# Kernel tuning notes

Hardware: AMD Instinct MI355X
Metric: run time of the kernel (lower is better)

## Reference

```python
import jax, jax.numpy as jnp
import numpy as np

T, D_MODEL, D_FF, N_EXPERTS, TOPK = 4096, 2048, 8192, 8, 2


def setup_inputs() -> dict:
    key = jax.random.key(0)
    k1, k2, k3, k4 = jax.random.split(key, 4)
    x = jax.random.normal(k1, (T, D_MODEL), dtype=jnp.float32)
    gating_output = jax.random.normal(k2, (T, N_EXPERTS), dtype=jnp.float32)
    # gate_proj and up_proj concatenated along output dim: [E, 2*d_ff, d_model]
    gate_up_proj = jax.random.normal(k3, (N_EXPERTS, 2 * D_FF, D_MODEL), dtype=jnp.float32) * 0.02
    # down_proj: [E, d_model, d_ff]
    down_proj = jax.random.normal(k4, (N_EXPERTS, D_MODEL, D_FF), dtype=jnp.float32) * 0.02
    return {"x": x, "gating_output": gating_output, "gate_up_proj": gate_up_proj,
            "down_proj": down_proj, "topk": TOPK}


def reference(x, gating_output, gate_up_proj, down_proj, topk):
    n_experts = gate_up_proj.shape[0]
    d_ff = down_proj.shape[2]
    # Router: fp32 softmax over experts, top-k, renormalize over the k selected.
    probs = jax.nn.softmax(gating_output.astype(jnp.float32), axis=1)  # [T, E]
    routing_weights, selected_experts = jax.lax.top_k(probs, topk)     # [T, k]
    routing_weights = routing_weights / jnp.sum(routing_weights, axis=-1, keepdims=True)
    routing_weights = routing_weights.astype(x.dtype)
    # Expert MLPs: silu(x @ Wg^T) * (x @ Wu^T) @ Wd^T, combined by routing weight.
    out = jnp.zeros_like(x)
    for e in range(n_experts):  # small fixed expert count
        coef = jnp.sum(jnp.where(selected_experts == e, routing_weights, 0.0), axis=-1)  # [T]
        gu = x @ gate_up_proj[e].T                     # [T, 2*d_ff]
        h = jax.nn.silu(gu[:, :d_ff]) * gu[:, d_ff:]   # [T, d_ff]
        out = out + coef[:, None] * (h @ down_proj[e].T)  # [T, d_model]
    return out
```

## Files before the change

### kernel.cpp

```cpp
#include <hip/hip_runtime.h>
#include <hip/hip_bf16.h>
#include <cstdint>
#include <cstddef>

#define T_TOK 4096
#define DMODEL 2048
#define DFF 8192
#define NEXP 8
#define NPAIR (T_TOK * 2)

typedef __bf16 bf16_t;
typedef __bf16 bf16x8 __attribute__((ext_vector_type(8)));
typedef float fx4 __attribute__((ext_vector_type(4)));

__device__ __forceinline__ void gload16(const bf16_t* src, bf16_t* dst) {
    __builtin_amdgcn_global_load_lds(
        (const __attribute__((address_space(1))) uint32_t*)(src),
        (__attribute__((address_space(3))) uint32_t*)(dst), 16, 0, 0);
}

__device__ __forceinline__ bf16x8 pack8(const fx4 lo, const fx4 hi) {
    bf16x8 o;
    o[0] = (bf16_t)lo[0]; o[1] = (bf16_t)lo[1]; o[2] = (bf16_t)lo[2]; o[3] = (bf16_t)lo[3];
    o[4] = (bf16_t)hi[0]; o[5] = (bf16_t)hi[1]; o[6] = (bf16_t)hi[2]; o[7] = (bf16_t)hi[3];
    return o;
}

__global__ void router_kernel(const float* __restrict__ gating, int* __restrict__ counts,
                              int* __restrict__ tok_list, float* __restrict__ w_list) {
    int t = blockIdx.x * blockDim.x + threadIdx.x;
    if (t >= T_TOK) return;
    float l[NEXP];
    float mx = -1e30f;
#pragma unroll
    for (int e = 0; e < NEXP; e++) { l[e] = gating[t * NEXP + e]; mx = fmaxf(mx, l[e]); }
#pragma unroll
    for (int e = 0; e < NEXP; e++) { l[e] = __expf(l[e] - mx); }
    int e0 = 0; float p0 = l[0];
#pragma unroll
    for (int e = 1; e < NEXP; e++) { if (l[e] > p0) { p0 = l[e]; e0 = e; } }
    int e1 = -1; float p1 = -1.0f;
#pragma unroll
    for (int e = 0; e < NEXP; e++) { if (e != e0 && l[e] > p1) { p1 = l[e]; e1 = e; } }
    float inv = 1.0f / (p0 + p1);
    int s0 = atomicAdd(&counts[e0], 1);
    tok_list[e0 * T_TOK + s0] = t; w_list[e0 * T_TOK + s0] = p0 * inv;
    int s1 = atomicAdd(&counts[e1], 1);
    tok_list[e1 * T_TOK + s1] = t; w_list[e1 * T_TOK + s1] = p1 * inv;
}

__global__ void scan_kernel(const int* __restrict__ counts, int* __restrict__ offsets) {
    if (threadIdx.x == 0 && blockIdx.x == 0) {
        int acc = 0;
        for (int e = 0; e < NEXP; e++) { offsets[e] = acc; acc += counts[e]; }
        offsets[NEXP] = acc;
    }
}

__global__ void cvt_x_kernel(const float* __restrict__ x, bf16_t* __restrict__ xb) {
    int i = blockIdx.x * blockDim.x + threadIdx.x;
    const fx4* src = (const fx4*)x;
    fx4 v0 = src[2 * i], v1 = src[2 * i + 1];
    *(bf16x8*)(xb + (size_t)i * 8) = pack8(v0, v1);
}

__global__ __launch_bounds__(512, 4) void gateup_kernel(
    const bf16_t* __restrict__ xb, const float* __restrict__ gup,
    const int* __restrict__ counts, const int* __restrict__ offsets,
    const int* __restrict__ tok_list, bf16_t* __restrict__ h_buf)
{
    const int idx = blockIdx.x;
    const int q = idx & 7;
    const int mslot = (idx >> 3) & 15;
    const int g2 = idx >> 7;
    const int e = g2 >> 4;
    const int cnt = counts[e];
    const int mbase = mslot * 256;
    if (mbase >= cnt) return;
    const int y = q + 8 * (g2 & 15);
    const int nb = y * 64;
    const int off_e = offsets[e];

    __shared__ __align__(16) bf16_t lds_a[256 * 64];
    __shared__ __align__(16) bf16_t lds_w[128 * 64];

    const int tid = threadIdx.x;
    const int lane = tid & 63;
    const int w = tid >> 6;
    const int wm = (w >> 1) * 64;
    const int wc = (w & 1);

    const bf16_t* a_src[4];
    int a_doff[4];
#pragma unroll
    for (int j = 0; j < 4; j++) {
        int row = (w * 4 + j) * 8 + (lane >> 3);
        int cs = (lane & 7) ^ (row & 7);
        int slot = mbase + row;
        int tok = tok_list[e * T_TOK + (slot < cnt ? slot : cnt - 1)];
        a_src[j] = xb + (size_t)tok * DMODEL + cs * 8;
        a_doff[j] = (w * 4 + j) * 512;
    }
    const float* w_src[2];
    int w_st[2];
    const float* gup_e = gup + (size_t)e * (2 * DFF) * DMODEL;
#pragma unroll
    for (int t = 0; t < 2; t++) {
        int cid = t * 512 + tid;
        int row = cid >> 3, c = cid & 7;
        int grow = (row < 64) ? (nb + row) : (DFF + nb + (row - 64));
        w_src[t] = gup_e + (size_t)grow * DMODEL + c * 8;
        w_st[t] = row * 64 + ((c ^ (row & 7)) * 8);
    }

    fx4 accg[4][2] = {};
    fx4 accu[4][2] = {};

    for (int k0 = 0; k0 < DMODEL; k0 += 64) {
#pragma unroll
        for (int j = 0; j < 4; j++) gload16(a_src[j] + k0, &lds_a[a_doff[j]]);
#pragma unroll
        for (int t = 0; t < 2; t++) {
            fx4 lo = *(const fx4*)(w_src[t] + k0);
            fx4 hi = *(const fx4*)(w_src[t] + k0 + 4);
            *(bf16x8*)(&lds_w[w_st[t]]) = pack8(lo, hi);
        }
        __syncthreads();
#pragma unroll
        for (int kp = 0; kp < 2; kp++) {
            const int ke = kp * 4 + (lane >> 4);
            bf16x8 af[4], gf[2], uf[2];
#pragma unroll
            for (int m = 0; m < 4; m++) {
                int r = wm + m * 16 + (lane & 15);
                af[m] = *(const bf16x8*)(&lds_a[r * 64 + ((ke ^ (r & 7)) * 8)]);
            }
#pragma unroll
            for (int n = 0; n < 2; n++) {
                int r = wc * 32 + n * 16 + (lane & 15);
                gf[n] = *(const bf16x8*)(&lds_w[r * 64 + ((ke ^ (r & 7)) * 8)]);
                uf[n] = *(const bf16x8*)(&lds_w[(r + 64) * 64 + ((ke ^ (r & 7)) * 8)]);
            }
#pragma unroll
            for (int m = 0; m < 4; m++)
#pragma unroll
                for (int n = 0; n < 2; n++) {
                    accg[m][n] = __builtin_amdgcn_mfma_f32_16x16x32_bf16(af[m], gf[n], accg[m][n], 0, 0, 0);
                    accu[m][n] = __builtin_amdgcn_mfma_f32_16x16x32_bf16(af[m], uf[n], accu[m][n], 0, 0, 0);
                }
        }
        __syncthreads();
    }

    const int colbase = nb + wc * 32 + (lane & 15);
#pragma unroll
    for (int m = 0; m < 4; m++) {
        int rb = wm + m * 16 + ((lane >> 4) * 4);
#pragma unroll
        for (int j = 0; j < 4; j++) {
            int slot = mbase + rb + j;
            if (slot < cnt) {
                size_t hrow = (size_t)(off_e + slot);
#pragma unroll
                for (int n = 0; n < 2; n++) {
                    float g = accg[m][n][j];
                    float u = accu[m][n][j];
                    float hv = g * u / (1.0f + __expf(-g));
                    h_buf[hrow * DFF + colbase + n * 16] = (bf16_t)hv;
                }
            }
        }
    }
}

__global__ __launch_bounds__(512, 4) void down_kernel(
    const bf16_t* __restrict__ h_buf, const float* __restrict__ dwn,
    const int* __restrict__ counts, const int* __restrict__ offsets,
    const int* __restrict__ tok_list, const float* __restrict__ w_list,
    float* __restrict__ out)
{
    const int idx = blockIdx.x;
    const int q = idx & 7;
    const int mslot = (idx >> 3) & 15;
    const int rest = idx >> 7;
    const int pp = rest & 1;
    const int e = rest >> 1;
    const int cnt = counts[e];
    const int mbase = mslot * 256;
    if (mbase >= cnt) return;
    const int y = q + 8 * pp;
    const int nbase = y * 128;
    const int off_e = offsets[e];

    __shared__ __align__(16) bf16_t lds_a[256 * 64];
    __shared__ __align__(16) bf16_t lds_w[128 * 64];

    const int tid = threadIdx.x;
    const int lane = tid & 63;
    const int w = tid >> 6;
    const int wm = (w >> 1) * 64;
    const int wn = (w & 1) * 64;

    const bf16_t* a_src[4];
    int a_doff[4];
#pragma unroll
    for (int j = 0; j < 4; j++) {
        int row = (w * 4 + j) * 8 + (lane >> 3);
        int cs = (lane & 7) ^ (row & 7);
        int slot = mbase + row;
        int hrow = off_e + (slot < cnt ? slot : cnt - 1);
        a_src[j] = h_buf + (size_t)hrow * DFF + cs * 8;
        a_doff[j] = (w * 4 + j) * 512;
    }
    const float* w_src[2];
    int w_st[2];
    const float* dwn_e = dwn + (size_t)e * DMODEL * DFF;
#pragma unroll
    for (int t = 0; t < 2; t++) {
        int cid = t * 512 + tid;
        int row = cid >> 3, c = cid & 7;
        w_src[t] = dwn_e + (size_t)(nbase + row) * DFF + c * 8;
        w_st[t] = row * 64 + ((c ^ (row & 7)) * 8);
    }

    fx4 acc[4][4] = {};

    for (int k0 = 0; k0 < DFF; k0 += 64) {
#pragma unroll
        for (int j = 0; j < 4; j++) gload16(a_src[j] + k0, &lds_a[a_doff[j]]);
#pragma unroll
        for (int t = 0; t < 2; t++) {
            fx4 lo = *(const fx4*)(w_src[t] + k0);
            fx4 hi = *(const fx4*)(w_src[t] + k0 + 4);
            *(bf16x8*)(&lds_w[w_st[t]]) = pack8(lo, hi);
        }
        __syncthreads();
#pragma unroll
        for (int kp = 0; kp < 2; kp++) {
            const int ke = kp * 4 + (lane >> 4);
            bf16x8 af[4], bfr[4];
#pragma unroll
            for (int m = 0; m < 4; m++) {
                int r = wm + m * 16 + (lane & 15);
                af[m] = *(const bf16x8*)(&lds_a[r * 64 + ((ke ^ (r & 7)) * 8)]);
            }
#pragma unroll
            for (int n = 0; n < 4; n++) {
                int r = wn + n * 16 + (lane & 15);
                bfr[n] = *(const bf16x8*)(&lds_w[r * 64 + ((ke ^ (r & 7)) * 8)]);
            }
#pragma unroll
            for (int m = 0; m < 4; m++)
#pragma unroll
                for (int n = 0; n < 4; n++)
                    acc[m][n] = __builtin_amdgcn_mfma_f32_16x16x32_bf16(af[m], bfr[n], acc[m][n], 0, 0, 0);
        }
        __syncthreads();
    }

    const int colb = nbase + wn + (lane & 15);
#pragma unroll
    for (int m = 0; m < 4; m++) {
        int rb = wm + m * 16 + ((lane >> 4) * 4);
#pragma unroll
        for (int j = 0; j < 4; j++) {
            int slot = mbase + rb + j;
            if (slot < cnt) {
                int tok = tok_list[e * T_TOK + slot];
                float wgt = w_list[e * T_TOK + slot];
#pragma unroll
                for (int n = 0; n < 4; n++)
                    atomicAdd(&out[(size_t)tok * DMODEL + colb + n * 16], wgt * acc[m][n][j]);
            }
        }
    }
}

extern "C" void kernel_launch(void* const* d_in, const int* in_sizes, int n_in,
                              void* d_out, int out_size, void* d_ws, size_t ws_size,
                              hipStream_t stream) {
    const float* x      = (const float*)d_in[0];
    const float* gating = (const float*)d_in[1];
    const float* gup    = (const float*)d_in[2];
    const float* dwn    = (const float*)d_in[3];
    float* out = (float*)d_out;

    char* ws = (char*)d_ws;
    int*    counts   = (int*)(ws + 0);
    int*    offsets  = (int*)(ws + 64);
    int*    tok_list = (int*)(ws + 128);
    float*  w_list   = (float*)(ws + 128 + 131072);
    bf16_t* xb       = (bf16_t*)(ws + 262400);
    bf16_t* h_buf    = (bf16_t*)(ws + 17039872);

    hipMemsetAsync(counts, 0, 64, stream);
    hipMemsetAsync(out, 0, (size_t)out_size * sizeof(float), stream);

    router_kernel<<<dim3(T_TOK / 256), dim3(256), 0, stream>>>(gating, counts, tok_list, w_list);
    scan_kernel<<<dim3(1), dim3(64), 0, stream>>>(counts, offsets);
    cvt_x_kernel<<<dim3(T_TOK * DMODEL / 8 / 256), dim3(256), 0, stream>>>(x, xb);

    gateup_kernel<<<dim3(16384), dim3(512), 0, stream>>>(
        xb, gup, counts, offsets, tok_list, h_buf);

    down_kernel<<<dim3(2048), dim3(512), 0, stream>>>(
        h_buf, dwn, counts, offsets, tok_list, w_list, out);
}
```

Baseline: 1.442 ms.

## Double-buffer LDS tiles and halve M-tile to 128 rows in MoE GEMMs

Both expert GEMM kernels now use 256-thread blocks with a 128-row M tile, and twice the blocks are launched. They ping-pong between two LDS buffers: the next k-tile's weights are prefetched into registers and the activations sent to LDS asynchronously while MFMAs run on the current tile. This is meant to hide global-load latency and cut one barrier per k-step. The cost is that each weight tile, converted from fp32, is now re-read by twice as many M-blocks, and register pressure rises from the prefetch buffers.

```diff
diff --git a/kernel.cpp b/kernel.cpp
--- a/kernel.cpp
+++ b/kernel.cpp
@@ -64,25 +64,25 @@
     *(bf16x8*)(xb + (size_t)i * 8) = pack8(v0, v1);
 }
 
-__global__ __launch_bounds__(512, 4) void gateup_kernel(
+__global__ __launch_bounds__(256, 2) void gateup_kernel(
     const bf16_t* __restrict__ xb, const float* __restrict__ gup,
     const int* __restrict__ counts, const int* __restrict__ offsets,
     const int* __restrict__ tok_list, bf16_t* __restrict__ h_buf)
 {
     const int idx = blockIdx.x;
     const int q = idx & 7;
-    const int mslot = (idx >> 3) & 15;
-    const int g2 = idx >> 7;
+    const int mslot = (idx >> 3) & 31;
+    const int g2 = idx >> 8;
     const int e = g2 >> 4;
     const int cnt = counts[e];
-    const int mbase = mslot * 256;
+    const int mbase = mslot * 128;
     if (mbase >= cnt) return;
     const int y = q + 8 * (g2 & 15);
     const int nb = y * 64;
     const int off_e = offsets[e];
 
-    __shared__ __align__(16) bf16_t lds_a[256 * 64];
-    __shared__ __align__(16) bf16_t lds_w[128 * 64];
+    __shared__ __align__(16) bf16_t lds_a[2][128 * 64];
+    __shared__ __align__(16) bf16_t lds_w[2][128 * 64];
 
     const int tid = threadIdx.x;
     const int lane = tid & 63;
@@ -101,31 +101,53 @@
         a_src[j] = xb + (size_t)tok * DMODEL + cs * 8;
         a_doff[j] = (w * 4 + j) * 512;
     }
-    const float* w_src[2];
-    int w_st[2];
+    const float* w_src[4];
+    int w_st[4];
     const float* gup_e = gup + (size_t)e * (2 * DFF) * DMODEL;
 #pragma unroll
-    for (int t = 0; t < 2; t++) {
-        int cid = t * 512 + tid;
+    for (int c4 = 0; c4 < 4; c4++) {
+        int cid = c4 * 256 + tid;
         int row = cid >> 3, c = cid & 7;
         int grow = (row < 64) ? (nb + row) : (DFF + nb + (row - 64));
-        w_src[t] = gup_e + (size_t)grow * DMODEL + c * 8;
-        w_st[t] = row * 64 + ((c ^ (row & 7)) * 8);
+        w_src[c4] = gup_e + (size_t)grow * DMODEL + c * 8;
+        w_st[c4] = row * 64 + ((c ^ (row & 7)) * 8);
     }
 
     fx4 accg[4][2] = {};
     fx4 accu[4][2] = {};
 
-    for (int k0 = 0; k0 < DMODEL; k0 += 64) {
-#pragma unroll
-        for (int j = 0; j < 4; j++) gload16(a_src[j] + k0, &lds_a[a_doff[j]]);
-#pragma unroll
-        for (int t = 0; t < 2; t++) {
-            fx4 lo = *(const fx4*)(w_src[t] + k0);
-            fx4 hi = *(const fx4*)(w_src[t] + k0 + 4);
-            *(bf16x8*)(&lds_w[w_st[t]]) = pack8(lo, hi);
-        }
+    {
+        fx4 wr[8];
+#pragma unroll
+        for (int c4 = 0; c4 < 4; c4++) {
+            wr[2 * c4]     = *(const fx4*)(w_src[c4]);
+            wr[2 * c4 + 1] = *(const fx4*)(w_src[c4] + 4);
+        }
+#pragma unroll
+        for (int j = 0; j < 4; j++) gload16(a_src[j], &lds_a[0][a_doff[j]]);
+#pragma unroll
+        for (int c4 = 0; c4 < 4; c4++)
+            *(bf16x8*)(&lds_w[0][w_st[c4]]) = pack8(wr[2 * c4], wr[2 * c4 + 1]);
         __syncthreads();
+    }
+
+    const int NT = DMODEL / 64;
+    for (int t = 0; t < NT; ++t) {
+        const int cur = t & 1;
+        const int nxt = cur ^ 1;
+        fx4 wr[8];
+        if (t + 1 < NT) {
+#pragma unroll
+            for (int c4 = 0; c4 < 4; c4++) {
+                wr[2 * c4]     = *(const fx4*)(w_src[c4] + (t + 1) * 64);
+                wr[2 * c4 + 1] = *(const fx4*)(w_src[c4] + (t + 1) * 64 + 4);
+            }
+#pragma unroll
+            for (int j = 0; j < 4; j++)
+                gload16(a_src[j] + (t + 1) * 64, &lds_a[nxt][a_doff[j]]);
+        }
+        const bf16_t* A = lds_a[cur];
+        const bf16_t* W = lds_w[cur];
 #pragma unroll
         for (int kp = 0; kp < 2; kp++) {
             const int ke = kp * 4 + (lane >> 4);
@@ -133,13 +155,13 @@
 #pragma unroll
             for (int m = 0; m < 4; m++) {
                 int r = wm + m * 16 + (lane & 15);
-                af[m] = *(const bf16x8*)(&lds_a[r * 64 + ((ke ^ (r & 7)) * 8)]);
+                af[m] = *(const bf16x8*)(&A[r * 64 + ((ke ^ (r & 7)) * 8)]);
             }
 #pragma unroll
             for (int n = 0; n < 2; n++) {
                 int r = wc * 32 + n * 16 + (lane & 15);
-                gf[n] = *(const bf16x8*)(&lds_w[r * 64 + ((ke ^ (r & 7)) * 8)]);
-                uf[n] = *(const bf16x8*)(&lds_w[(r + 64) * 64 + ((ke ^ (r & 7)) * 8)]);
+                gf[n] = *(const bf16x8*)(&W[r * 64 + ((ke ^ (r & 7)) * 8)]);
+                uf[n] = *(const bf16x8*)(&W[(r + 64) * 64 + ((ke ^ (r & 7)) * 8)]);
             }
 #pragma unroll
             for (int m = 0; m < 4; m++)
@@ -148,6 +170,11 @@
                     accg[m][n] = __builtin_amdgcn_mfma_f32_16x16x32_bf16(af[m], gf[n], accg[m][n], 0, 0, 0);
                     accu[m][n] = __builtin_amdgcn_mfma_f32_16x16x32_bf16(af[m], uf[n], accu[m][n], 0, 0, 0);
                 }
+        }
+        if (t + 1 < NT) {
+#pragma unroll
+            for (int c4 = 0; c4 < 4; c4++)
+                *(bf16x8*)(&lds_w[nxt][w_st[c4]]) = pack8(wr[2 * c4], wr[2 * c4 + 1]);
         }
         __syncthreads();
     }
@@ -173,7 +200,7 @@
     }
 }
 
-__global__ __launch_bounds__(512, 4) void down_kernel(
+__global__ __launch_bounds__(256, 2) void down_kernel(
     const bf16_t* __restrict__ h_buf, const float* __restrict__ dwn,
     const int* __restrict__ counts, const int* __restrict__ offsets,
     const int* __restrict__ tok_list, const float* __restrict__ w_list,
@@ -181,19 +208,19 @@
 {
     const int idx = blockIdx.x;
     const int q = idx & 7;
-    const int mslot = (idx >> 3) & 15;
-    const int rest = idx >> 7;
+    const int mslot = (idx >> 3) & 31;
+    const int rest = idx >> 8;
     const int pp = rest & 1;
     const int e = rest >> 1;
     const int cnt = counts[e];
-    const int mbase = mslot * 256;
+    const int mbase = mslot * 128;
     if (mbase >= cnt) return;
     const int y = q + 8 * pp;
     const int nbase = y * 128;
     const int off_e = offsets[e];
 
-    __shared__ __align__(16) bf16_t lds_a[256 * 64];
-    __shared__ __align__(16) bf16_t lds_w[128 * 64];
+    __shared__ __align__(16) bf16_t lds_a[2][128 * 64];
+    __shared__ __align__(16) bf16_t lds_w[2][128 * 64];
 
     const int tid = threadIdx.x;
     const int lane = tid & 63;
@@ -212,29 +239,51 @@
         a_src[j] = h_buf + (size_t)hrow * DFF + cs * 8;
         a_doff[j] = (w * 4 + j) * 512;
     }
-    const float* w_src[2];
-    int w_st[2];
+    const float* w_src[4];
+    int w_st[4];
     const float* dwn_e = dwn + (size_t)e * DMODEL * DFF;
 #pragma unroll
-    for (int t = 0; t < 2; t++) {
-        int cid = t * 512 + tid;
+    for (int c4 = 0; c4 < 4; c4++) {
+        int cid = c4 * 256 + tid;
         int row = cid >> 3, c = cid & 7;
-        w_src[t] = dwn_e + (size_t)(nbase + row) * DFF + c * 8;
-        w_st[t] = row * 64 + ((c ^ (row & 7)) * 8);
+        w_src[c4] = dwn_e + (size_t)(nbase + row) * DFF + c * 8;
+        w_st[c4] = row * 64 + ((c ^ (row & 7)) * 8);
     }
 
     fx4 acc[4][4] = {};
 
-    for (int k0 = 0; k0 < DFF; k0 += 64) {
-#pragma unroll
-        for (int j = 0; j < 4; j++) gload16(a_src[j] + k0, &lds_a[a_doff[j]]);
-#pragma unroll
-        for (int t = 0; t < 2; t++) {
-            fx4 lo = *(const fx4*)(w_src[t] + k0);
-            fx4 hi = *(const fx4*)(w_src[t] + k0 + 4);
-            *(bf16x8*)(&lds_w[w_st[t]]) = pack8(lo, hi);
-        }
+    {
+        fx4 wr[8];
+#pragma unroll
+        for (int c4 = 0; c4 < 4; c4++) {
+            wr[2 * c4]     = *(const fx4*)(w_src[c4]);
+            wr[2 * c4 + 1] = *(const fx4*)(w_src[c4] + 4);
+        }
+#pragma unroll
+        for (int j = 0; j < 4; j++) gload16(a_src[j], &lds_a[0][a_doff[j]]);
+#pragma unroll
+        for (int c4 = 0; c4 < 4; c4++)
+            *(bf16x8*)(&lds_w[0][w_st[c4]]) = pack8(wr[2 * c4], wr[2 * c4 + 1]);
         __syncthreads();
+    }
+
+    const int NT = DFF / 64;
+    for (int t = 0; t < NT; ++t) {
+        const int cur = t & 1;
+        const int nxt = cur ^ 1;
+        fx4 wr[8];
+        if (t + 1 < NT) {
+#pragma unroll
+            for (int c4 = 0; c4 < 4; c4++) {
+                wr[2 * c4]     = *(const fx4*)(w_src[c4] + (t + 1) * 64);
+                wr[2 * c4 + 1] = *(const fx4*)(w_src[c4] + (t + 1) * 64 + 4);
+            }
+#pragma unroll
+            for (int j = 0; j < 4; j++)
+                gload16(a_src[j] + (t + 1) * 64, &lds_a[nxt][a_doff[j]]);
+        }
+        const bf16_t* A = lds_a[cur];
+        const bf16_t* W = lds_w[cur];
 #pragma unroll
         for (int kp = 0; kp < 2; kp++) {
             const int ke = kp * 4 + (lane >> 4);
@@ -242,18 +291,23 @@
 #pragma unroll
             for (int m = 0; m < 4; m++) {
                 int r = wm + m * 16 + (lane & 15);
-                af[m] = *(const bf16x8*)(&lds_a[r * 64 + ((ke ^ (r & 7)) * 8)]);
+                af[m] = *(const bf16x8*)(&A[r * 64 + ((ke ^ (r & 7)) * 8)]);
             }
 #pragma unroll
             for (int n = 0; n < 4; n++) {
                 int r = wn + n * 16 + (lane & 15);
-                bfr[n] = *(const bf16x8*)(&lds_w[r * 64 + ((ke ^ (r & 7)) * 8)]);
+                bfr[n] = *(const bf16x8*)(&W[r * 64 + ((ke ^ (r & 7)) * 8)]);
             }
 #pragma unroll
             for (int m = 0; m < 4; m++)
 #pragma unroll
                 for (int n = 0; n < 4; n++)
                     acc[m][n] = __builtin_amdgcn_mfma_f32_16x16x32_bf16(af[m], bfr[n], acc[m][n], 0, 0, 0);
+        }
+        if (t + 1 < NT) {
+#pragma unroll
+            for (int c4 = 0; c4 < 4; c4++)
+                *(bf16x8*)(&lds_w[nxt][w_st[c4]]) = pack8(wr[2 * c4], wr[2 * c4 + 1]);
         }
         __syncthreads();
     }
@@ -300,9 +354,9 @@
     scan_kernel<<<dim3(1), dim3(64), 0, stream>>>(counts, offsets);
     cvt_x_kernel<<<dim3(T_TOK * DMODEL / 8 / 256), dim3(256), 0, stream>>>(x, xb);
 
-    gateup_kernel<<<dim3(16384), dim3(512), 0, stream>>>(
+    gateup_kernel<<<dim3(32768), dim3(256), 0, stream>>>(
         xb, gup, counts, offsets, tok_list, h_buf);
 
-    down_kernel<<<dim3(2048), dim3(512), 0, stream>>>(
+    down_kernel<<<dim3(4096), dim3(256), 0, stream>>>(
         h_buf, dwn, counts, offsets, tok_list, w_list, out);
 }
```

New measurement: 1.849 ms. 28.2% more time.

## Pre-convert expert weights to bf16 and use async LDS loads in GEMMs

Applied to the files above, without the earlier changes.

Adds a kernel that converts the fp32 gate/up and down weights to bf16 in workspace on every call. New GEMM kernels then stream the bf16 weights straight into LDS with global_load_lds, using 128-row M tiles and 256-thread blocks instead of 256-row tiles and 512 threads. The aim is to drop the in-loop fp32 weight conversion and simplify the load path. In exchange, each call pays an extra full read and write of the weights. The new path runs only when the workspace is large enough; otherwise the old fp32 kernels are kept as a fallback.

```diff
diff --git a/kernel.cpp b/kernel.cpp
--- a/kernel.cpp
+++ b/kernel.cpp
@@ -64,7 +64,226 @@
     *(bf16x8*)(xb + (size_t)i * 8) = pack8(v0, v1);
 }
 
-__global__ __launch_bounds__(512, 4) void gateup_kernel(
+__global__ void wcvt_kernel(const float* __restrict__ src, bf16_t* __restrict__ dst, int nchunk) {
+    int stride = gridDim.x * blockDim.x;
+    for (int i = blockIdx.x * blockDim.x + threadIdx.x; i < nchunk; i += stride) {
+        const fx4* s = (const fx4*)src + 2 * (size_t)i;
+        fx4 v0 = s[0], v1 = s[1];
+        *(bf16x8*)(dst + (size_t)i * 8) = pack8(v0, v1);
+    }
+}
+
+__global__ __launch_bounds__(256, 4) void gateup_kernel(
+    const bf16_t* __restrict__ xb, const bf16_t* __restrict__ wg,
+    const int* __restrict__ counts, const int* __restrict__ offsets,
+    const int* __restrict__ tok_list, bf16_t* __restrict__ h_buf)
+{
+    const int idx = blockIdx.x;
+    const int q = idx & 7;
+    const int mslot = (idx >> 3) & 31;
+    const int g2 = idx >> 8;
+    const int e = g2 >> 4;
+    const int cnt = counts[e];
+    const int mbase = mslot * 128;
+    if (mbase >= cnt) return;
+    const int y = q + 8 * (g2 & 15);
+    const int nb = y * 64;
+    const int off_e = offsets[e];
+
+    __shared__ __align__(16) bf16_t lds_a[128 * 64];
+    __shared__ __align__(16) bf16_t lds_w[128 * 64];
+
+    const int tid = threadIdx.x;
+    const int lane = tid & 63;
+    const int w = tid >> 6;
+    const int wm = (w >> 1) * 64;
+    const int wc = (w & 1);
+    const int l15 = lane & 15;
+    const int l4 = lane >> 4;
+
+    const bf16_t* a_src[4];
+    int a_doff[4];
+#pragma unroll
+    for (int j = 0; j < 4; j++) {
+        int row = (w * 4 + j) * 8 + (lane >> 3);
+        int c8 = (lane & 7) ^ (row & 7);
+        int slot = mbase + row;
+        int tok = tok_list[e * T_TOK + (slot < cnt ? slot : cnt - 1)];
+        a_src[j] = xb + (size_t)tok * DMODEL + c8 * 8;
+        a_doff[j] = (w * 4 + j) * 512;
+    }
+    const bf16_t* w_src[4];
+    int w_doff[4];
+    const bf16_t* wg_e = wg + (size_t)e * (2 * DFF) * DMODEL;
+#pragma unroll
+    for (int j = 0; j < 4; j++) {
+        int row = (w * 4 + j) * 8 + (lane >> 3);
+        int c8 = (lane & 7) ^ (row & 7);
+        int grow = (row < 64) ? (nb + row) : (DFF + nb + (row - 64));
+        w_src[j] = wg_e + (size_t)grow * DMODEL + c8 * 8;
+        w_doff[j] = (w * 4 + j) * 512;
+    }
+
+    fx4 accg[4][2] = {};
+    fx4 accu[4][2] = {};
+
+    for (int k0 = 0; k0 < DMODEL; k0 += 64) {
+#pragma unroll
+        for (int j = 0; j < 4; j++) {
+            gload16(a_src[j] + k0, &lds_a[a_doff[j]]);
+            gload16(w_src[j] + k0, &lds_w[w_doff[j]]);
+        }
+        __syncthreads();
+#pragma unroll
+        for (int kp = 0; kp < 2; kp++) {
+            const int ke = kp * 4 + l4;
+            bf16x8 af[4], gf[2], uf[2];
+#pragma unroll
+            for (int m = 0; m < 4; m++) {
+                int r = wm + m * 16 + l15;
+                af[m] = *(const bf16x8*)(&lds_a[r * 64 + ((ke ^ (r & 7)) * 8)]);
+            }
+#pragma unroll
+            for (int n = 0; n < 2; n++) {
+                int r = wc * 32 + n * 16 + l15;
+                gf[n] = *(const bf16x8*)(&lds_w[r * 64 + ((ke ^ (r & 7)) * 8)]);
+                uf[n] = *(const bf16x8*)(&lds_w[(r + 64) * 64 + (((ke) ^ ((r + 64) & 7)) * 8)]);
+            }
+#pragma unroll
+            for (int m = 0; m < 4; m++)
+#pragma unroll
+                for (int n = 0; n < 2; n++) {
+                    accg[m][n] = __builtin_amdgcn_mfma_f32_16x16x32_bf16(af[m], gf[n], accg[m][n], 0, 0, 0);
+                    accu[m][n] = __builtin_amdgcn_mfma_f32_16x16x32_bf16(af[m], uf[n], accu[m][n], 0, 0, 0);
+                }
+        }
+        __syncthreads();
+    }
+
+    const int colbase = nb + wc * 32 + l15;
+#pragma unroll
+    for (int m = 0; m < 4; m++) {
+        int rb = wm + m * 16 + l4 * 4;
+#pragma unroll
+        for (int j = 0; j < 4; j++) {
+            int slot = mbase + rb + j;
+            if (slot < cnt) {
+                size_t hrow = (size_t)(off_e + slot);
+#pragma unroll
+                for (int n = 0; n < 2; n++) {
+                    float g = accg[m][n][j];
+                    float u = accu[m][n][j];
+                    float hv = g * u / (1.0f + __expf(-g));
+                    h_buf[hrow * DFF + colbase + n * 16] = (bf16_t)hv;
+                }
+            }
+        }
+    }
+}
+
+__global__ __launch_bounds__(256, 4) void down_kernel(
+    const bf16_t* __restrict__ h_buf, const bf16_t* __restrict__ wd,
+    const int* __restrict__ counts, const int* __restrict__ offsets,
+    const int* __restrict__ tok_list, const float* __restrict__ w_list,
+    float* __restrict__ out)
+{
+    const int idx = blockIdx.x;
+    const int q = idx & 7;
+    const int mslot = (idx >> 3) & 31;
+    const int rest = idx >> 8;
+    const int pp = rest & 1;
+    const int e = rest >> 1;
+    const int cnt = counts[e];
+    const int mbase = mslot * 128;
+    if (mbase >= cnt) return;
+    const int y = q + 8 * pp;
+    const int nbase = y * 128;
+    const int off_e = offsets[e];
+
+    __shared__ __align__(16) bf16_t lds_a[128 * 64];
+    __shared__ __align__(16) bf16_t lds_w[128 * 64];
+
+    const int tid = threadIdx.x;
+    const int lane = tid & 63;
+    const int w = tid >> 6;
+    const int wm = (w >> 1) * 64;
+    const int wn = (w & 1) * 64;
+    const int l15 = lane & 15;
+    const int l4 = lane >> 4;
+
+    const bf16_t* a_src[4];
+    int a_doff[4];
+#pragma unroll
+    for (int j = 0; j < 4; j++) {
+        int row = (w * 4 + j) * 8 + (lane >> 3);
+        int c8 = (lane & 7) ^ (row & 7);
+        int slot = mbase + row;
+        int hrow = off_e + (slot < cnt ? slot : cnt - 1);
+        a_src[j] = h_buf + (size_t)hrow * DFF + c8 * 8;
+        a_doff[j] = (w * 4 + j) * 512;
+    }
+    const bf16_t* w_src[4];
+    int w_doff[4];
+    const bf16_t* wd_e = wd + (size_t)e * DMODEL * DFF;
+#pragma unroll
+    for (int j = 0; j < 4; j++) {
+        int row = (w * 4 + j) * 8 + (lane >> 3);
+        int c8 = (lane & 7) ^ (row & 7);
+        w_src[j] = wd_e + (size_t)(nbase + row) * DFF + c8 * 8;
+        w_doff[j] = (w * 4 + j) * 512;
+    }
+
+    fx4 acc[4][4] = {};
+
+    for (int k0 = 0; k0 < DFF; k0 += 64) {
+#pragma unroll
+        for (int j = 0; j < 4; j++) {
+            gload16(a_src[j] + k0, &lds_a[a_doff[j]]);
+            gload16(w_src[j] + k0, &lds_w[w_doff[j]]);
+        }
+        __syncthreads();
+#pragma unroll
+        for (int kp = 0; kp < 2; kp++) {
+            const int ke = kp * 4 + l4;
+            bf16x8 af[4], bfr[4];
+#pragma unroll
+            for (int m = 0; m < 4; m++) {
+                int r = wm + m * 16 + l15;
+                af[m] = *(const bf16x8*)(&lds_a[r * 64 + ((ke ^ (r & 7)) * 8)]);
+            }
+#pragma unroll
+            for (int n = 0; n < 4; n++) {
+                int r = wn + n * 16 + l15;
+                bfr[n] = *(const bf16x8*)(&lds_w[r * 64 + ((ke ^ (r & 7)) * 8)]);
+            }
+#pragma unroll
+            for (int m = 0; m < 4; m++)
+#pragma unroll
+                for (int n = 0; n < 4; n++)
+                    acc[m][n] = __builtin_amdgcn_mfma_f32_16x16x32_bf16(af[m], bfr[n], acc[m][n], 0, 0, 0);
+        }
+        __syncthreads();
+    }
+
+    const int colb = nbase + wn + l15;
+#pragma unroll
+    for (int m = 0; m < 4; m++) {
+        int rb = wm + m * 16 + l4 * 4;
+#pragma unroll
+        for (int j = 0; j < 4; j++) {
+            int slot = mbase + rb + j;
+            if (slot < cnt) {
+                int tok = tok_list[e * T_TOK + slot];
+                float wgt = w_list[e * T_TOK + slot];
+#pragma unroll
+                for (int n = 0; n < 4; n++)
+                    atomicAdd(&out[(size_t)tok * DMODEL + colb + n * 16], wgt * acc[m][n][j]);
+            }
+        }
+    }
+}
+
+__global__ __launch_bounds__(512, 4) void gateup_f32_kernel(
     const bf16_t* __restrict__ xb, const float* __restrict__ gup,
     const int* __restrict__ counts, const int* __restrict__ offsets,
     const int* __restrict__ tok_list, bf16_t* __restrict__ h_buf)
@@ -173,7 +392,7 @@
     }
 }
 
-__global__ __launch_bounds__(512, 4) void down_kernel(
+__global__ __launch_bounds__(512, 4) void down_f32_kernel(
     const bf16_t* __restrict__ h_buf, const float* __restrict__ dwn,
     const int* __restrict__ counts, const int* __restrict__ offsets,
     const int* __restrict__ tok_list, const float* __restrict__ w_list,
@@ -292,6 +511,9 @@
     float*  w_list   = (float*)(ws + 128 + 131072);
     bf16_t* xb       = (bf16_t*)(ws + 262400);
     bf16_t* h_buf    = (bf16_t*)(ws + 17039872);
+    bf16_t* wg_b     = (bf16_t*)(ws + 151257600);
+    bf16_t* wd_b     = (bf16_t*)(ws + 688128512);
+    const size_t WS_NEED = 956563968ull;
 
     hipMemsetAsync(counts, 0, 64, stream);
     hipMemsetAsync(out, 0, (size_t)out_size * sizeof(float), stream);
@@ -300,9 +522,18 @@
     scan_kernel<<<dim3(1), dim3(64), 0, stream>>>(counts, offsets);
     cvt_x_kernel<<<dim3(T_TOK * DMODEL / 8 / 256), dim3(256), 0, stream>>>(x, xb);
 
-    gateup_kernel<<<dim3(16384), dim3(512), 0, stream>>>(
-        xb, gup, counts, offsets, tok_list, h_buf);
-
-    down_kernel<<<dim3(2048), dim3(512), 0, stream>>>(
-        h_buf, dwn, counts, offsets, tok_list, w_list, out);
-}
+    if (ws_size >= WS_NEED) {
+        wcvt_kernel<<<dim3(2048), dim3(256), 0, stream>>>(gup, wg_b, NEXP * 2 * DFF * DMODEL / 8);
+        wcvt_kernel<<<dim3(2048), dim3(256), 0, stream>>>(dwn, wd_b, NEXP * DMODEL * DFF / 8);
+
+        gateup_kernel<<<dim3(32768), dim3(256), 0, stream>>>(
+            xb, wg_b, counts, offsets, tok_list, h_buf);
+        down_kernel<<<dim3(4096), dim3(256), 0, stream>>>(
+            h_buf, wd_b, counts, offsets, tok_list, w_list, out);
+    } else {
+        gateup_f32_kernel<<<dim3(16384), dim3(512), 0, stream>>>(
+            xb, gup, counts, offsets, tok_list, h_buf);
+        down_f32_kernel<<<dim3(2048), dim3(512), 0, stream>>>(
+            h_buf, dwn, counts, offsets, tok_list, w_list, out);
+    }
+}
```

Measured after the change: 2.896 ms. +100.9%, slower.
